# Kernel tuning notes

Measured on AMD Instinct MI355X. Metric: run time of the kernel, lower is better.

The kernel has to match this reference:

```python
import jax, jax.numpy as jnp
import numpy as np

HEAD = 8
K_DIM = 64
ROUNDS = 4
BUCKETS = 32
ACN = 1  # attend_chunk_num
SELF_VAL = -100000.0


def across(x, acn=ACN):
    """Concatenate each chunk with its acn left/right neighbor chunks (wrapping).
    x: (..., n_chunks, chunk_size, feat). Rolls along chunk axis (-3), cats along -2.
    Order matches the torch code: left chunks, self, right chunks."""
    shifts = list(range(acn, 0, -1)) + [0] + list(range(-1, -acn - 1, -1))
    return jnp.concatenate([jnp.roll(x, s, axis=-3) for s in shifts], axis=-2)


def gather_seq(src, idx):
    """src: (b,h,s,f); idx: (b,h,r,s) -> (b,h,r,s,f) (per-round permutation gather)."""
    return jnp.take_along_axis(src[:, :, None, :, :], idx[..., None], axis=-2)


def lsh_forward(x, Wq, bq, Wv, bv, Wo, bo, hash_vec):
    b, s, d = x.shape
    h, k, r = HEAD, K_DIM, ROUNDS
    qk = (x @ Wq + bq).reshape(b, s, h, k).transpose(0, 2, 1, 3)  # (b,h,s,k)
    v = (x @ Wv + bv).reshape(b, s, h, k).transpose(0, 2, 1, 3)   # (b,h,s,k)

    # --- LSH hashing: argmax over [-rot, rot] rotations ---
    rot = jnp.einsum('bhsk,hkvr->bhsvr', qk, hash_vec)
    rot = jnp.concatenate([-rot, rot], axis=-2)
    buckets = jnp.argmax(rot, axis=-2).transpose(0, 1, 3, 2)  # (b,h,r,s)

    ticker = jnp.arange(s)
    buckets = buckets * s + ticker  # stable-sort key: bucket major, position minor
    s_ticker = jnp.argsort(buckets, axis=-1)
    s_buckets = jnp.take_along_axis(buckets, s_ticker, axis=-1)
    undo = jnp.argsort(s_ticker, axis=-1)

    s_qk = gather_seq(qk, s_ticker)  # (b,h,r,s,k)
    s_v = gather_seq(v, s_ticker)
    nrm = jnp.maximum(jnp.linalg.norm(s_qk, axis=-1, keepdims=True), 1e-12)
    s_k = s_qk / nrm  # F.normalize(p=2)

    nb = BUCKETS
    cs = s // nb
    cq = s_qk.reshape(b, h, r, nb, cs, k)
    ck = s_k.reshape(b, h, r, nb, cs, k)
    cv = s_v.reshape(b, h, r, nb, cs, k)
    ct = s_ticker.reshape(b, h, r, nb, cs)

    ak = across(ck)                      # (b,h,r,nb,3cs,k)
    av = across(cv)
    at = across(ct[..., None])[..., 0]   # (b,h,r,nb,3cs)

    dots = jnp.einsum('bhrnik,bhrnjk->bhrnij', cq, ak) * (k ** -0.5)
    NEG = -jnp.finfo(dots.dtype).max

    # self-attention penalty mask
    dots = jnp.where(ct[..., :, None] == at[..., None, :], SELF_VAL, dots)

    # different-bucket mask
    bid = (s_buckets // s).reshape(b, h, r, nb, cs)
    abid = across(bid[..., None])[..., 0]
    dots = jnp.where(bid[..., :, None] != abid[..., None, :], NEG, dots)

    # duplicate count across rounds (same bucket id in any round)
    loc = (buckets // s).transpose(0, 1, 3, 2)     # (b,h,s,r)
    s_loc = gather_seq(loc, s_ticker)              # (b,h,r,s,r)
    cl = s_loc.reshape(b, h, r, nb, cs, r)
    al = across(cl)                                # (b,h,r,nb,3cs,r)
    dup = (cl[..., :, None, :] == al[..., None, :, :]).sum(-1).astype(dots.dtype)
    dup = jax.lax.stop_gradient(dup)
    dots = dots - jnp.log(dup + 1e-9)

    lse = jax.nn.logsumexp(dots, axis=-1, keepdims=True)
    p = jnp.exp(dots - lse)
    vo = jnp.einsum('bhrnij,bhrnjk->bhrnik', p, av).reshape(b, h, r, s, k)
    lse = lse.reshape(b, h, r, s)

    # unsort back to original token order
    vo = jnp.take_along_axis(vo, undo[..., None], axis=-2)
    lse = jnp.take_along_axis(lse, undo, axis=-1)

    # combine rounds with softmax over per-round logsumexp
    w = jnp.exp(lse - jax.nn.logsumexp(lse, axis=2, keepdims=True))
    out = (vo * w[..., None]).sum(axis=2)  # (b,h,s,k)
    out = out.transpose(0, 2, 1, 3).reshape(b, s, h * k)
    return out @ Wo + bo  # dropout is identity in eval


def setup_inputs() -> dict:
    key = jax.random.key(0)
    ks = jax.random.split(key, 8)
    b, s, d = 2, 2048, 512
    sc = 1.0 / np.sqrt(d)  # keep activations numerically tame
    return {
        'x': jax.random.normal(ks[0], (b, s, d), jnp.float32),
        'Wq': jax.random.normal(ks[1], (d, d), jnp.float32) * sc,
        'bq': jax.random.normal(ks[2], (d,), jnp.float32) * 0.01,
        'Wv': jax.random.normal(ks[3], (d, d), jnp.float32) * sc,
        'bv': jax.random.normal(ks[4], (d,), jnp.float32) * 0.01,
        'Wo': jax.random.normal(ks[5], (d, d), jnp.float32) * sc,
        'bo': jax.random.normal(ks[6], (d,), jnp.float32) * 0.01,
        'hash_vec': jax.random.normal(ks[7], (HEAD, K_DIM, BUCKETS // 2, ROUNDS), jnp.float32),
    }


def reference(x, Wq, bq, Wv, bv, Wo, bo, hash_vec):
    return lsh_forward(x, Wq, bq, Wv, bv, Wo, bo, hash_vec)
```

## Files before the change

kernel.cpp:

```cpp
#include <hip/hip_runtime.h>
#include <hip/hip_bf16.h>
#include <math.h>

#define WS_ 192
#define NEGF (-3.402823466e+38f)

typedef __attribute__((ext_vector_type(8))) short short8;
typedef __attribute__((ext_vector_type(4))) float f32x4;
typedef __attribute__((ext_vector_type(4))) unsigned int u32x4;

static __device__ __forceinline__ unsigned int f2bf(float f) {
    unsigned int u = __float_as_uint(f);
    return (u + 0x7FFFu + ((u >> 16) & 1u)) >> 16;
}
static __device__ __forceinline__ unsigned int packsplit(float v) {
    unsigned int h = f2bf(v);
    float hf = __uint_as_float(h << 16);
    unsigned int l = f2bf(v - hf);
    return h | (l << 16);
}
static __device__ __forceinline__ void mkfrag(uint4 a, uint4 b, short8 &h, short8 &l) {
    u32x4 hv, lv;
    hv[0] = __builtin_amdgcn_perm(a.y, a.x, 0x05040100u);
    hv[1] = __builtin_amdgcn_perm(a.w, a.z, 0x05040100u);
    hv[2] = __builtin_amdgcn_perm(b.y, b.x, 0x05040100u);
    hv[3] = __builtin_amdgcn_perm(b.w, b.z, 0x05040100u);
    lv[0] = __builtin_amdgcn_perm(a.y, a.x, 0x07060302u);
    lv[1] = __builtin_amdgcn_perm(a.w, a.z, 0x07060302u);
    lv[2] = __builtin_amdgcn_perm(b.y, b.x, 0x07060302u);
    lv[3] = __builtin_amdgcn_perm(b.w, b.z, 0x07060302u);
    h = __builtin_bit_cast(short8, hv);
    l = __builtin_bit_cast(short8, lv);
}
static __device__ __forceinline__ unsigned int cvtpk(float lo, float hi) {
    unsigned int d;
    asm("v_cvt_pk_bf16_f32 %0, %1, %2" : "=v"(d) : "v"(lo), "v"(hi));
    return d;
}
static __device__ __forceinline__ void gload_lds16(const void* g, void* l) {
    __builtin_amdgcn_global_load_lds(
        (const __attribute__((address_space(1))) void*)g,
        (__attribute__((address_space(3))) void*)l, 16, 0, 0);
}

__global__ __launch_bounds__(256) void prep_kernel(const float* __restrict__ A,
                                                   const float* __restrict__ W,
                                                   const float* __restrict__ bias,
                                                   const float* __restrict__ hv,
                                                   const float* __restrict__ Wv,
                                                   const float* __restrict__ Wo,
                                                   unsigned short* __restrict__ qkr,
                                                   float* __restrict__ scaleQ,
                                                   int* __restrict__ loc2,
                                                   unsigned int* __restrict__ xpk,
                                                   unsigned int* __restrict__ wvT,
                                                   unsigned int* __restrict__ woT) {
    __shared__ float BUF[4352];
    const int bid = blockIdx.x;
    const int tid = threadIdx.x;

    if (bid >= 512) {
        int pb = bid - 512;
        if (pb < 2048) {
            int idx = (pb * 256 + tid) * 4;
            float4 v = *(const float4*)(A + idx);
            uint4 pk = make_uint4(packsplit(v.x), packsplit(v.y),
                                  packsplit(v.z), packsplit(v.w));
            *(uint4*)(xpk + idx) = pk;
            return;
        }
        unsigned int* T = (unsigned int*)BUF;
        int wb = pb - 2048;
        const float* Wsrc = (wb < 64) ? Wv : Wo;
        unsigned int* Wdst = (wb < 64) ? wvT : woT;
        int t = wb & 63;
        int k0 = (t >> 3) * 64, n0 = (t & 7) * 64;
#pragma unroll
        for (int pass = 0; pass < 16; ++pass) {
            int i = pass * 4 + (tid >> 6);
            int j = tid & 63;
            T[j * 65 + i] = packsplit(Wsrc[(size_t)(k0 + i) * 512 + n0 + j]);
        }
        __syncthreads();
#pragma unroll
        for (int pass = 0; pass < 16; ++pass) {
            int j = pass * 4 + (tid >> 6);
            int i = tid & 63;
            Wdst[(size_t)(n0 + j) * 512 + k0 + i] = T[j * 65 + i];
        }
        return;
    }

    float* As = BUF;
    float* Ws = BUF + 2176;
    const int m0 = (bid & 63) * 64;
    const int n0 = (bid >> 6) * 64;
    const int ty = tid >> 4, tx = tid & 15;
    const int ci = tid & 7, ri = tid >> 3;
    const int wk = tid >> 4, wt = tid & 15;
    float acc[4][4] = {};
    for (int k0 = 0; k0 < 512; k0 += 32) {
#pragma unroll
        for (int h2 = 0; h2 < 2; ++h2) {
            int i = ri + h2 * 32;
            float4 a4 = *(const float4*)(A + (size_t)(m0 + i) * 512 + k0 + ci * 4);
            As[(ci * 4 + 0) * 68 + i] = a4.x;
            As[(ci * 4 + 1) * 68 + i] = a4.y;
            As[(ci * 4 + 2) * 68 + i] = a4.z;
            As[(ci * 4 + 3) * 68 + i] = a4.w;
        }
#pragma unroll
        for (int h2 = 0; h2 < 2; ++h2) {
            int kk = wk + h2 * 16;
            float4 w4 = *(const float4*)(W + (size_t)(k0 + kk) * 512 + n0 + wt * 4);
            *(float4*)(&Ws[kk * 68 + wt * 4]) = w4;
        }
        __syncthreads();
#pragma unroll
        for (int kk = 0; kk < 32; ++kk) {
            float4 a4 = *(float4*)(&As[kk * 68 + ty * 4]);
            float4 w4 = *(float4*)(&Ws[kk * 68 + tx * 4]);
            float a[4] = {a4.x, a4.y, a4.z, a4.w};
            float w[4] = {w4.x, w4.y, w4.z, w4.w};
#pragma unroll
            for (int i = 0; i < 4; ++i)
#pragma unroll
                for (int j = 0; j < 4; ++j) acc[i][j] += a[i] * w[j];
        }
        __syncthreads();
    }
    const int hh = n0 >> 6;
#pragma unroll
    for (int i = 0; i < 4; ++i) {
        int m = m0 + ty * 4 + i;
        int b = m >> 11, s = m & 2047;
        float v0 = acc[i][0] + bias[n0 + tx * 4 + 0];
        float v1 = acc[i][1] + bias[n0 + tx * 4 + 1];
        float v2 = acc[i][2] + bias[n0 + tx * 4 + 2];
        float v3 = acc[i][3] + bias[n0 + tx * 4 + 3];
        acc[i][0] = v0; acc[i][1] = v1; acc[i][2] = v2; acc[i][3] = v3;
        unsigned int h0 = f2bf(v0), h1 = f2bf(v1), h2v = f2bf(v2), h3 = f2bf(v3);
        unsigned int l0 = f2bf(v0 - __uint_as_float(h0 << 16));
        unsigned int l1 = f2bf(v1 - __uint_as_float(h1 << 16));
        unsigned int l2 = f2bf(v2 - __uint_as_float(h2v << 16));
        unsigned int l3 = f2bf(v3 - __uint_as_float(h3 << 16));
        size_t trow = ((size_t)(((b << 3) + hh) * 2048 + s)) * 128;
        *(uint2*)(qkr + trow + tx * 4) =
            make_uint2(h0 | (h1 << 16), h2v | (h3 << 16));
        *(uint2*)(qkr + trow + 64 + tx * 4) =
            make_uint2(l0 | (l1 << 16), l2 | (l3 << 16));
        float sq = v0 * v0 + v1 * v1 + v2 * v2 + v3 * v3;
        sq += __shfl_xor(sq, 1, 16); sq += __shfl_xor(sq, 2, 16);
        sq += __shfl_xor(sq, 4, 16); sq += __shfl_xor(sq, 8, 16);
        if (tx == 0)
            scaleQ[(size_t)(((b << 3) + hh) * 2048 + s)] = 0.125f / fmaxf(sqrtf(sq), 1e-12f);
    }
#pragma unroll
    for (int j = 0; j < 4; ++j) {
        int f = tx * 4 + j;
        int xm = (f & 7) << 3;
#pragma unroll
        for (int i = 0; i < 4; ++i)
            BUF[f * 68 + ((ty * 4 + i) ^ xm)] = acc[i][j];
    }
    __syncthreads();
    const float* hvb = hv + (size_t)hh * 4096 + tx * 4;
    float rt[4][4] = {};
#pragma unroll 4
    for (int f = 0; f < 64; ++f) {
        float4 q4 = *(float4*)(&BUF[f * 68 + ((ty * 4) ^ ((f & 7) << 3))]);
        float4 h4 = *(const float4*)(hvb + f * 64);
        float q[4] = {q4.x, q4.y, q4.z, q4.w};
        float hw[4] = {h4.x, h4.y, h4.z, h4.w};
#pragma unroll
        for (int i = 0; i < 4; ++i)
#pragma unroll
            for (int j = 0; j < 4; ++j) rt[i][j] += q[i] * hw[j];
    }
    __syncthreads();
#pragma unroll
    for (int i = 0; i < 4; ++i)
        *(float4*)(&BUF[(ty * 4 + i) * 68 + tx * 4]) =
            make_float4(rt[i][0], rt[i][1], rt[i][2], rt[i][3]);
    __syncthreads();
    {
        const int tok = tid >> 2, rr2 = tid & 3;
        float best = -BUF[tok * 68 + rr2];
        int bj = 0;
        for (int j = 1; j < 16; ++j) {
            float v = BUF[tok * 68 + j * 4 + rr2];
            if (-v > best) { best = -v; bj = j; }
        }
        for (int j = 0; j < 16; ++j) {
            float v = BUF[tok * 68 + j * 4 + rr2];
            if (v > best) { best = v; bj = 16 + j; }
        }
        int m = m0 + tok;
        int b = m >> 11, s = m & 2047;
        loc2[((size_t)(((b << 3) + hh) * 2048 + s)) * 4 + rr2] = bj;
    }
}

__global__ __launch_bounds__(256) void gemm_pk(const unsigned int* __restrict__ Apk,
                                               const unsigned int* __restrict__ BT,
                                               const float* __restrict__ bias,
                                               void* __restrict__ Cout, int mode) {
    __shared__ __align__(16) unsigned int As[64 * 32];
    __shared__ __align__(16) unsigned int Bs[64 * 32];
    const int m0 = blockIdx.x * 64;
    const int n0 = blockIdx.y * 64;
    const int tid = threadIdx.x;
    const int lane = tid & 63, wv = tid >> 6;
    const int lx = lane & 15, hi = lane >> 4;
    const int wbase = tid & ~63;
    f32x4 acc[4] = {{0.f,0.f,0.f,0.f},{0.f,0.f,0.f,0.f},{0.f,0.f,0.f,0.f},{0.f,0.f,0.f,0.f}};
    for (int k0 = 0; k0 < 512; k0 += 32) {
#pragma unroll
        for (int u = 0; u < 2; ++u) {
            int qi = u * 256 + tid;
            int row = qi >> 3, qd = qi & 7;
            int sq = (qd ^ (row & 7)) << 2;
            gload_lds16(Apk + (size_t)(m0 + row) * 512 + k0 + sq,
                        &As[(u * 256 + wbase) * 4]);
            gload_lds16(BT + (size_t)(n0 + row) * 512 + k0 + sq,
                        &Bs[(u * 256 + wbase) * 4]);
        }
        __syncthreads();
        int arow = wv * 16 + lx;
        uint4 a0 = *(uint4*)(&As[arow * 32 + (((2 * hi) ^ (arow & 7)) << 2)]);
        uint4 a1 = *(uint4*)(&As[arow * 32 + (((2 * hi + 1) ^ (arow & 7)) << 2)]);
        short8 Ah, Al; mkfrag(a0, a1, Ah, Al);
#pragma unroll
        for (int j = 0; j < 4; ++j) {
            int brow = j * 16 + lx;
            uint4 b0 = *(uint4*)(&Bs[brow * 32 + (((2 * hi) ^ (brow & 7)) << 2)]);
            uint4 b1 = *(uint4*)(&Bs[brow * 32 + (((2 * hi + 1) ^ (brow & 7)) << 2)]);
            short8 Bh2, Bl2; mkfrag(b0, b1, Bh2, Bl2);
            acc[j] = __builtin_amdgcn_mfma_f32_16x16x32_bf16(Ah, Bh2, acc[j], 0, 0, 0);
            acc[j] = __builtin_amdgcn_mfma_f32_16x16x32_bf16(Ah, Bl2, acc[j], 0, 0, 0);
            acc[j] = __builtin_amdgcn_mfma_f32_16x16x32_bf16(Al, Bh2, acc[j], 0, 0, 0);
        }
        __syncthreads();
    }
#pragma unroll
    for (int j = 0; j < 4; ++j) {
        int nn = n0 + j * 16 + lx;
        float bs = bias[nn];
#pragma unroll
        for (int reg = 0; reg < 4; ++reg) {
            int m = m0 + wv * 16 + hi * 4 + reg;
            float val = acc[j][reg] + bs;
            if (mode == 0) {
                int b = m >> 11, ss = m & 2047;
                int hh = nn >> 6, f = nn & 63;
                ((unsigned short*)Cout)[((size_t)(((b << 3) + hh) * 2048 + ss)) * 64 + f] =
                    (unsigned short)f2bf(val);
            } else {
                ((float*)Cout)[(size_t)m * 512 + nn] = val;
            }
        }
    }
}

__global__ __launch_bounds__(1024) void sort_kernel(const int* __restrict__ loc2,
                                                    int* __restrict__ st) {
    __shared__ int hist[32][32];
    __shared__ int off[32][32];
    __shared__ int base[32];
    const int gid = blockIdx.x;
    const int r = gid & 3, bh = gid >> 2;
    const int tid = threadIdx.x;
    const int lane = tid & 63, wvi = tid >> 6;
    const unsigned long long lower_mask =
        (lane == 0) ? 0ull : ((~0ull) >> (64 - lane));

    int myb[2], myrank[2];
#pragma unroll
    for (int si = 0; si < 2; ++si) {
        int seg = wvi * 2 + si;
        int p = seg * 64 + lane;
        int b = loc2[(size_t)(bh * 2048 + p) * 4 + r];
        myb[si] = b;
        myrank[si] = 0;
#pragma unroll 1
        for (int bkt = 0; bkt < 32; ++bkt) {
            unsigned long long m = __ballot(b == bkt);
            if (b == bkt) myrank[si] = __popcll(m & lower_mask);
            if (lane == bkt) hist[seg][bkt] = __popcll(m);
        }
    }
    __syncthreads();
    if (tid < 32) {
        int running = 0;
#pragma unroll 1
        for (int seg = 0; seg < 32; ++seg) {
            off[seg][tid] = running;
            running += hist[seg][tid];
        }
        base[tid] = running;
    }
    __syncthreads();
    if (tid == 0) {
        int acc = 0;
#pragma unroll 1
        for (int b = 0; b < 32; ++b) { int h = base[b]; base[b] = acc; acc += h; }
    }
    __syncthreads();
#pragma unroll
    for (int si = 0; si < 2; ++si) {
        int seg = wvi * 2 + si;
        int p = seg * 64 + lane;
        int b = myb[si];
        st[(size_t)gid * 2048 + base[b] + off[seg][b] + myrank[si]] = p;
    }
}

#define KSLOT(row, sl) (((row) << 6) + ((((sl) ^ ((row) & 15))) << 2))
#define PBASE 6400

__global__ __launch_bounds__(256, 3) void attn_kernel(const unsigned short* __restrict__ qkr,
                                                      const unsigned short* __restrict__ vpk,
                                                      const float* __restrict__ scaleQ,
                                                      const int* __restrict__ loc2,
                                                      const int* __restrict__ st,
                                                      float* __restrict__ lseg,
                                                      float* __restrict__ vog) {
    __shared__ __align__(16) unsigned int U[12800];
    __shared__ float scaleK[WS_];
    __shared__ int Tk[WS_];
    __shared__ int Lp[WS_];

    const int gid = blockIdx.x;
    const int n = gid & 31;
    const int r = (gid >> 5) & 3;
    const int bh = gid >> 7;
    const int tid = threadIdx.x;
    const int sbase = (bh * 4 + r) * 2048;
    const int lane = tid & 63;
    const int wv = tid >> 6;
    const int lx = lane & 15;
    const int hi = lane >> 4;

    if (tid < WS_) {
        int w = tid;
        int chunk = (n + 31 + (w >> 6)) & 31;
        int t = st[(size_t)sbase + chunk * 64 + (w & 63)];
        Tk[w] = t;
        int4 l4 = *(const int4*)(loc2 + (size_t)(bh * 2048 + t) * 4);
        Lp[w] = l4.x | (l4.y << 8) | (l4.z << 16) | (l4.w << 24);
        scaleK[w] = scaleQ[bh * 2048 + t];
    }
    __syncthreads();

#pragma unroll
    for (int it = 0; it < 12; ++it) {
        int s = it * 256 + tid;
        int row = s >> 4, sl = s & 15;
        uint4 v4 = *(const uint4*)(qkr + ((size_t)(bh * 2048 + Tk[row])) * 128 + sl * 8);
        *(uint4*)(&U[KSLOT(row, sl)]) = v4;
    }
    __syncthreads();

    const int qw = 64 + wv * 16 + lx;
    short8 Bh[2], Bl[2];
#pragma unroll
    for (int ks = 0; ks < 2; ++ks) {
        Bh[ks] = __builtin_bit_cast(short8, *(uint4*)(&U[KSLOT(qw, ks * 4 + hi)]));
        Bl[ks] = __builtin_bit_cast(short8, *(uint4*)(&U[KSLOT(qw, 8 + ks * 4 + hi)]));
    }
    f32x4 s[12];
    __builtin_amdgcn_s_setprio(1);
#pragma unroll
    for (int ct = 0; ct < 12; ++ct) {
        f32x4 acc = {0.f, 0.f, 0.f, 0.f};
#pragma unroll
        for (int ks = 0; ks < 2; ++ks) {
            int arow = ct * 16 + lx;
            short8 Ah = __builtin_bit_cast(short8, *(uint4*)(&U[KSLOT(arow, ks * 4 + hi)]));
            short8 Al = __builtin_bit_cast(short8, *(uint4*)(&U[KSLOT(arow, 8 + ks * 4 + hi)]));
            acc = __builtin_amdgcn_mfma_f32_16x16x32_bf16(Ah, Bh[ks], acc, 0, 0, 0);
            acc = __builtin_amdgcn_mfma_f32_16x16x32_bf16(Ah, Bl[ks], acc, 0, 0, 0);
            acc = __builtin_amdgcn_mfma_f32_16x16x32_bf16(Al, Bh[ks], acc, 0, 0, 0);
        }
        s[ct] = acc;
    }
    __builtin_amdgcn_s_setprio(0);

    uint4 vl0[3], vl1[3];
#pragma unroll
    for (int it = 0; it < 3; ++it) {
        int idx = it * 256 + tid;
        int pr = idx >> 3, oct = idx & 7;
        vl0[it] = *(const uint4*)(vpk + ((size_t)(bh * 2048 + Tk[pr * 2])) * 64 + oct * 8);
        vl1[it] = *(const uint4*)(vpk + ((size_t)(bh * 2048 + Tk[pr * 2 + 1])) * 64 + oct * 8);
    }
    __syncthreads();

    const int lq = Lp[qw];
    const unsigned int bmask = 0x80u << (r * 8);
    float mx = -3.0e38f;
#pragma unroll
    for (int ct = 0; ct < 12; ++ct) {
#pragma unroll
        for (int rr = 0; rr < 4; ++rr) {
            int c = ct * 16 + hi * 4 + rr;
            float val = s[ct][rr] * scaleK[c];
            unsigned int x = (unsigned int)(lq ^ Lp[c]);
            unsigned int z = ((x & 0x7f7f7f7fu) + 0x7f7f7f7fu) | x;
            unsigned int zm = ~z & 0x80808080u;
            int dup = __popc(zm);
            val = (c == qw) ? -100000.0f : val;
            val = (zm & bmask) ? val : NEGF;
            float ld = (dup < 2) ? 0.0f
                     : (dup == 2) ? 0.69314718f
                     : (dup == 3) ? 1.09861229f : 1.38629436f;
            val -= ld;
            s[ct][rr] = val;
            mx = fmaxf(mx, val);
        }
    }
    mx = fmaxf(mx, __shfl_xor(mx, 16));
    mx = fmaxf(mx, __shfl_xor(mx, 32));
    float ssum = 0.f;
#pragma unroll
    for (int ct = 0; ct < 12; ++ct)
#pragma unroll
        for (int rr = 0; rr < 4; ++rr) {
            float e = __expf(s[ct][rr] - mx);
            s[ct][rr] = e;
            ssum += e;
        }
    ssum += __shfl_xor(ssum, 16);
    ssum += __shfl_xor(ssum, 32);
    float lse = mx + __logf(ssum);
    if (hi == 0) lseg[(size_t)sbase + Tk[qw]] = lse;
    float inv = 1.0f / ssum;

#pragma unroll
    for (int it = 0; it < 3; ++it) {
        int idx = it * 256 + tid;
        int pr = idx >> 3, oct = idx & 7;
        int c0 = pr * 2;
        unsigned int aw[4] = {vl0[it].x, vl0[it].y, vl0[it].z, vl0[it].w};
        unsigned int bw[4] = {vl1[it].x, vl1[it].y, vl1[it].z, vl1[it].w};
#pragma unroll
        for (int j = 0; j < 8; ++j) {
            int f = oct * 8 + j;
            unsigned int w2 = (j & 1)
                ? __builtin_amdgcn_perm(bw[j >> 1], aw[j >> 1], 0x07060302u)
                : __builtin_amdgcn_perm(bw[j >> 1], aw[j >> 1], 0x05040100u);
            int quad = (c0 >> 3) ^ (f & 7) ^ (f >> 3);
            U[f * 100 + (quad << 2) + ((c0 & 7) >> 1)] = w2;
        }
    }
    const int q = wv * 16 + lx;
    const int pxm = (q & 3) << 3;
#pragma unroll
    for (int ct = 0; ct < 12; ++ct) {
        int po = ct * 8 + hi * 2;
        U[PBASE + q * 100 + ((po + 0) ^ pxm)] = cvtpk(s[ct][0] * inv, s[ct][1] * inv);
        U[PBASE + q * 100 + ((po + 1) ^ pxm)] = cvtpk(s[ct][2] * inv, s[ct][3] * inv);
    }
    __syncthreads();

    f32x4 o[4] = {{0.f,0.f,0.f,0.f},{0.f,0.f,0.f,0.f},{0.f,0.f,0.f,0.f},{0.f,0.f,0.f,0.f}};
    const unsigned short* Uh = (const unsigned short*)U;
    __builtin_amdgcn_s_setprio(1);
#pragma unroll
    for (int ks = 0; ks < 6; ++ks) {
        short8 P8 = *(const short8*)(Uh + PBASE * 2 + q * 200 +
                                     (((ks * 16 + hi * 4) ^ pxm) << 1));
#pragma unroll
        for (int ft = 0; ft < 4; ++ft) {
            int f = ft * 16 + lx;
            int quad = (4 * ks + hi) ^ (f & 7) ^ (f >> 3);
            short8 V8 = *(const short8*)(Uh + f * 200 + (quad << 3));
            o[ft] = __builtin_amdgcn_mfma_f32_16x16x32_bf16(V8, P8, o[ft], 0, 0, 0);
        }
    }
    __builtin_amdgcn_s_setprio(0);
    const int tko = Tk[qw];
#pragma unroll
    for (int ft = 0; ft < 4; ++ft) {
        float4 w4 = make_float4(o[ft][0], o[ft][1], o[ft][2], o[ft][3]);
        *(float4*)(vog + ((size_t)sbase + tko) * 64 + ft * 16 + hi * 4) = w4;
    }
}

__global__ __launch_bounds__(256) void combine_kernel(const float* __restrict__ vog,
                                                      const float* __restrict__ lseg,
                                                      unsigned int* __restrict__ attpk) {
    const int gid = blockIdx.x * 256 + threadIdx.x;
    const int kq = gid & 15;
    const int t = (gid >> 4) & 2047;
    const int bh = gid >> 15;
    const int b = bh >> 3, h = bh & 7;
    float l[4];
    float4 vo[4];
#pragma unroll
    for (int r = 0; r < 4; ++r) {
        l[r] = lseg[(size_t)(bh * 4 + r) * 2048 + t];
        vo[r] = *(const float4*)(vog + ((size_t)(bh * 4 + r) * 2048 + t) * 64 + kq * 4);
    }
    float m = fmaxf(fmaxf(l[0], l[1]), fmaxf(l[2], l[3]));
    float ss = expf(l[0] - m) + expf(l[1] - m) + expf(l[2] - m) + expf(l[3] - m);
    float lt = m + logf(ss);
    float o0 = 0.f, o1 = 0.f, o2 = 0.f, o3 = 0.f;
#pragma unroll
    for (int r = 0; r < 4; ++r) {
        float w = expf(l[r] - lt);
        o0 += w * vo[r].x; o1 += w * vo[r].y; o2 += w * vo[r].z; o3 += w * vo[r].w;
    }
    uint4 pk = make_uint4(packsplit(o0), packsplit(o1), packsplit(o2), packsplit(o3));
    *(uint4*)(attpk + ((size_t)(b * 2048 + t)) * 512 + h * 64 + kq * 4) = pk;
}

extern "C" void kernel_launch(void* const* d_in, const int* in_sizes, int n_in,
                              void* d_out, int out_size, void* d_ws, size_t ws_size,
                              hipStream_t stream) {
    const float* x  = (const float*)d_in[0];
    const float* Wq = (const float*)d_in[1];
    const float* bq = (const float*)d_in[2];
    const float* Wv = (const float*)d_in[3];
    const float* bv = (const float*)d_in[4];
    const float* Wo = (const float*)d_in[5];
    const float* bo = (const float*)d_in[6];
    const float* hv = (const float*)d_in[7];

    unsigned int* W = (unsigned int*)d_ws;
    float*          vog    = (float*)W;
    unsigned int*   xpk    = W + 2097152;
    unsigned short* qkr    = (unsigned short*)(W + 8388608);
    unsigned short* vpk    = (unsigned short*)(W + 10485760);
    unsigned int*   attpk  = W + 11534336;
    float*          scaleQ = (float*)(W + 13631488);
    int*            loc2   = (int*)(W + 13664256);
    int*            stbuf  = (int*)(W + 13795328);
    float*          lseg   = (float*)(W + 13926400);
    unsigned int*   wvT    = W + 14057472;
    unsigned int*   woT    = W + 14319616;

    dim3 gg(64, 8), blk(256);
    prep_kernel<<<2688, 256, 0, stream>>>(x, Wq, bq, hv, Wv, Wo,
                                          qkr, scaleQ, loc2, xpk, wvT, woT);
    gemm_pk<<<gg, blk, 0, stream>>>(xpk, wvT, bv, (void*)vpk, 0);
    sort_kernel<<<64, 1024, 0, stream>>>(loc2, stbuf);
    attn_kernel<<<2048, 256, 0, stream>>>(qkr, vpk, scaleQ, loc2, stbuf, lseg, vog);
    combine_kernel<<<2048, 256, 0, stream>>>(vog, lseg, attpk);
    gemm_pk<<<gg, blk, 0, stream>>>(attpk, woT, bo, d_out, 1);
}
```

Before: 146.8 us.

## Store split-bf16 operands as separate hi/lo planes and fuse sort into V GEMM

The packed hi|lo bf16 layout for x, Wv, Wo and the attention output becomes two separate planes per row (hi in the first 512 entries, lo in the next 512). The GEMM can then load MFMA fragments directly from LDS without per-fragment byte permutes. The bucket counting sort moves from its own kernel into the V-projection GEMM launch as extra blocks, saving one launch and letting the sort overlap the GEMM. The cost is that each sort block now handles 8 segments per wave with 256 threads instead of 1024.

```diff
diff --git a/kernel.cpp b/kernel.cpp
--- a/kernel.cpp
+++ b/kernel.cpp
@@ -7,7 +7,6 @@
 
 typedef __attribute__((ext_vector_type(8))) short short8;
 typedef __attribute__((ext_vector_type(4))) float f32x4;
-typedef __attribute__((ext_vector_type(4))) unsigned int u32x4;
 
 static __device__ __forceinline__ unsigned int f2bf(float f) {
     unsigned int u = __float_as_uint(f);
@@ -18,19 +17,6 @@
     float hf = __uint_as_float(h << 16);
     unsigned int l = f2bf(v - hf);
     return h | (l << 16);
-}
-static __device__ __forceinline__ void mkfrag(uint4 a, uint4 b, short8 &h, short8 &l) {
-    u32x4 hv, lv;
-    hv[0] = __builtin_amdgcn_perm(a.y, a.x, 0x05040100u);
-    hv[1] = __builtin_amdgcn_perm(a.w, a.z, 0x05040100u);
-    hv[2] = __builtin_amdgcn_perm(b.y, b.x, 0x05040100u);
-    hv[3] = __builtin_amdgcn_perm(b.w, b.z, 0x05040100u);
-    lv[0] = __builtin_amdgcn_perm(a.y, a.x, 0x07060302u);
-    lv[1] = __builtin_amdgcn_perm(a.w, a.z, 0x07060302u);
-    lv[2] = __builtin_amdgcn_perm(b.y, b.x, 0x07060302u);
-    lv[3] = __builtin_amdgcn_perm(b.w, b.z, 0x07060302u);
-    h = __builtin_bit_cast(short8, hv);
-    l = __builtin_bit_cast(short8, lv);
 }
 static __device__ __forceinline__ unsigned int cvtpk(float lo, float hi) {
     unsigned int d;
@@ -52,9 +38,9 @@
                                                    unsigned short* __restrict__ qkr,
                                                    float* __restrict__ scaleQ,
                                                    int* __restrict__ loc2,
-                                                   unsigned int* __restrict__ xpk,
-                                                   unsigned int* __restrict__ wvT,
-                                                   unsigned int* __restrict__ woT) {
+                                                   unsigned short* __restrict__ xpk,
+                                                   unsigned short* __restrict__ wvT,
+                                                   unsigned short* __restrict__ woT) {
     __shared__ float BUF[4352];
     const int bid = blockIdx.x;
     const int tid = threadIdx.x;
@@ -63,16 +49,22 @@
         int pb = bid - 512;
         if (pb < 2048) {
             int idx = (pb * 256 + tid) * 4;
+            int row = idx >> 9, k = idx & 511;
             float4 v = *(const float4*)(A + idx);
-            uint4 pk = make_uint4(packsplit(v.x), packsplit(v.y),
-                                  packsplit(v.z), packsplit(v.w));
-            *(uint4*)(xpk + idx) = pk;
+            unsigned int h0 = f2bf(v.x), h1 = f2bf(v.y), h2 = f2bf(v.z), h3 = f2bf(v.w);
+            unsigned int l0 = f2bf(v.x - __uint_as_float(h0 << 16));
+            unsigned int l1 = f2bf(v.y - __uint_as_float(h1 << 16));
+            unsigned int l2 = f2bf(v.z - __uint_as_float(h2 << 16));
+            unsigned int l3 = f2bf(v.w - __uint_as_float(h3 << 16));
+            size_t rb = (size_t)row * 1024 + k;
+            *(uint2*)(xpk + rb)       = make_uint2(h0 | (h1 << 16), h2 | (h3 << 16));
+            *(uint2*)(xpk + rb + 512) = make_uint2(l0 | (l1 << 16), l2 | (l3 << 16));
             return;
         }
         unsigned int* T = (unsigned int*)BUF;
         int wb = pb - 2048;
         const float* Wsrc = (wb < 64) ? Wv : Wo;
-        unsigned int* Wdst = (wb < 64) ? wvT : woT;
+        unsigned short* Wdst = (wb < 64) ? wvT : woT;
         int t = wb & 63;
         int k0 = (t >> 3) * 64, n0 = (t & 7) * 64;
 #pragma unroll
@@ -86,7 +78,10 @@
         for (int pass = 0; pass < 16; ++pass) {
             int j = pass * 4 + (tid >> 6);
             int i = tid & 63;
-            Wdst[(size_t)(n0 + j) * 512 + k0 + i] = T[j * 65 + i];
+            unsigned int pk = T[j * 65 + i];
+            size_t rb = (size_t)(n0 + j) * 1024 + k0 + i;
+            Wdst[rb]       = (unsigned short)(pk & 0xffffu);
+            Wdst[rb + 512] = (unsigned short)(pk >> 16);
         }
         return;
     }
@@ -201,41 +196,99 @@
     }
 }
 
-__global__ __launch_bounds__(256) void gemm_pk(const unsigned int* __restrict__ Apk,
-                                               const unsigned int* __restrict__ BT,
+__global__ __launch_bounds__(256) void gemm_pk(const unsigned short* __restrict__ Apk,
+                                               const unsigned short* __restrict__ BT,
                                                const float* __restrict__ bias,
-                                               void* __restrict__ Cout, int mode) {
+                                               void* __restrict__ Cout, int mode,
+                                               const int* __restrict__ loc2,
+                                               int* __restrict__ st) {
     __shared__ __align__(16) unsigned int As[64 * 32];
     __shared__ __align__(16) unsigned int Bs[64 * 32];
-    const int m0 = blockIdx.x * 64;
-    const int n0 = blockIdx.y * 64;
+    const int bid = blockIdx.x;
     const int tid = threadIdx.x;
+
+    if (bid >= 512) {
+        int gid = bid - 512;
+        int r = gid & 3, bh = gid >> 2;
+        int* hist = (int*)As;
+        int* off  = (int*)As + 1024;
+        int* base = (int*)Bs;
+        const int lane = tid & 63, wvi = tid >> 6;
+        const unsigned long long lower_mask =
+            (lane == 0) ? 0ull : ((~0ull) >> (64 - lane));
+        int myb[8], myrank[8];
+#pragma unroll
+        for (int si = 0; si < 8; ++si) {
+            int seg = wvi * 8 + si;
+            int p = seg * 64 + lane;
+            int b = loc2[(size_t)(bh * 2048 + p) * 4 + r];
+            myb[si] = b;
+            myrank[si] = 0;
+#pragma unroll 1
+            for (int bkt = 0; bkt < 32; ++bkt) {
+                unsigned long long m = __ballot(b == bkt);
+                if (b == bkt) myrank[si] = __popcll(m & lower_mask);
+                if (lane == bkt) hist[seg * 32 + bkt] = __popcll(m);
+            }
+        }
+        __syncthreads();
+        if (tid < 32) {
+            int running = 0;
+#pragma unroll 1
+            for (int seg = 0; seg < 32; ++seg) {
+                off[seg * 32 + tid] = running;
+                running += hist[seg * 32 + tid];
+            }
+            base[tid] = running;
+        }
+        __syncthreads();
+        if (tid == 0) {
+            int a2 = 0;
+#pragma unroll 1
+            for (int b = 0; b < 32; ++b) { int h = base[b]; base[b] = a2; a2 += h; }
+        }
+        __syncthreads();
+#pragma unroll
+        for (int si = 0; si < 8; ++si) {
+            int seg = wvi * 8 + si;
+            int p = seg * 64 + lane;
+            int b = myb[si];
+            st[(size_t)gid * 2048 + base[b] + off[seg * 32 + b] + myrank[si]] = p;
+        }
+        return;
+    }
+
+    const int m0 = (bid & 63) * 64;
+    const int n0 = (bid >> 6) * 64;
     const int lane = tid & 63, wv = tid >> 6;
-    const int lx = lane & 15, hi = lane >> 4;
+    const int lx = lane & 15, fg = lane >> 4;
     const int wbase = tid & ~63;
     f32x4 acc[4] = {{0.f,0.f,0.f,0.f},{0.f,0.f,0.f,0.f},{0.f,0.f,0.f,0.f},{0.f,0.f,0.f,0.f}};
     for (int k0 = 0; k0 < 512; k0 += 32) {
 #pragma unroll
         for (int u = 0; u < 2; ++u) {
             int qi = u * 256 + tid;
-            int row = qi >> 3, qd = qi & 7;
-            int sq = (qd ^ (row & 7)) << 2;
-            gload_lds16(Apk + (size_t)(m0 + row) * 512 + k0 + sq,
+            int row = qi >> 3, sl = qi & 7;
+            int ssl = sl ^ (row & 7);
+            int offp = (ssl < 4) ? (k0 + ssl * 8) : (512 + k0 + (ssl - 4) * 8);
+            gload_lds16(Apk + (size_t)(m0 + row) * 1024 + offp,
                         &As[(u * 256 + wbase) * 4]);
-            gload_lds16(BT + (size_t)(n0 + row) * 512 + k0 + sq,
+            gload_lds16(BT + (size_t)(n0 + row) * 1024 + offp,
                         &Bs[(u * 256 + wbase) * 4]);
         }
         __syncthreads();
         int arow = wv * 16 + lx;
-        uint4 a0 = *(uint4*)(&As[arow * 32 + (((2 * hi) ^ (arow & 7)) << 2)]);
-        uint4 a1 = *(uint4*)(&As[arow * 32 + (((2 * hi + 1) ^ (arow & 7)) << 2)]);
-        short8 Ah, Al; mkfrag(a0, a1, Ah, Al);
+        short8 Ah = __builtin_bit_cast(short8,
+            *(uint4*)(&As[arow * 32 + ((fg ^ (arow & 7)) << 2)]));
+        short8 Al = __builtin_bit_cast(short8,
+            *(uint4*)(&As[arow * 32 + (((4 + fg) ^ (arow & 7)) << 2)]));
 #pragma unroll
         for (int j = 0; j < 4; ++j) {
             int brow = j * 16 + lx;
-            uint4 b0 = *(uint4*)(&Bs[brow * 32 + (((2 * hi) ^ (brow & 7)) << 2)]);
-            uint4 b1 = *(uint4*)(&Bs[brow * 32 + (((2 * hi + 1) ^ (brow & 7)) << 2)]);
-            short8 Bh2, Bl2; mkfrag(b0, b1, Bh2, Bl2);
+            short8 Bh2 = __builtin_bit_cast(short8,
+                *(uint4*)(&Bs[brow * 32 + ((fg ^ (brow & 7)) << 2)]));
+            short8 Bl2 = __builtin_bit_cast(short8,
+                *(uint4*)(&Bs[brow * 32 + (((4 + fg) ^ (brow & 7)) << 2)]));
             acc[j] = __builtin_amdgcn_mfma_f32_16x16x32_bf16(Ah, Bh2, acc[j], 0, 0, 0);
             acc[j] = __builtin_amdgcn_mfma_f32_16x16x32_bf16(Ah, Bl2, acc[j], 0, 0, 0);
             acc[j] = __builtin_amdgcn_mfma_f32_16x16x32_bf16(Al, Bh2, acc[j], 0, 0, 0);
@@ -248,7 +301,7 @@
         float bs = bias[nn];
 #pragma unroll
         for (int reg = 0; reg < 4; ++reg) {
-            int m = m0 + wv * 16 + hi * 4 + reg;
+            int m = m0 + wv * 16 + fg * 4 + reg;
             float val = acc[j][reg] + bs;
             if (mode == 0) {
                 int b = m >> 11, ss = m & 2047;
@@ -259,59 +312,6 @@
                 ((float*)Cout)[(size_t)m * 512 + nn] = val;
             }
         }
-    }
-}
-
-__global__ __launch_bounds__(1024) void sort_kernel(const int* __restrict__ loc2,
-                                                    int* __restrict__ st) {
-    __shared__ int hist[32][32];
-    __shared__ int off[32][32];
-    __shared__ int base[32];
-    const int gid = blockIdx.x;
-    const int r = gid & 3, bh = gid >> 2;
-    const int tid = threadIdx.x;
-    const int lane = tid & 63, wvi = tid >> 6;
-    const unsigned long long lower_mask =
-        (lane == 0) ? 0ull : ((~0ull) >> (64 - lane));
-
-    int myb[2], myrank[2];
-#pragma unroll
-    for (int si = 0; si < 2; ++si) {
-        int seg = wvi * 2 + si;
-        int p = seg * 64 + lane;
-        int b = loc2[(size_t)(bh * 2048 + p) * 4 + r];
-        myb[si] = b;
-        myrank[si] = 0;
-#pragma unroll 1
-        for (int bkt = 0; bkt < 32; ++bkt) {
-            unsigned long long m = __ballot(b == bkt);
-            if (b == bkt) myrank[si] = __popcll(m & lower_mask);
-            if (lane == bkt) hist[seg][bkt] = __popcll(m);
-        }
-    }
-    __syncthreads();
-    if (tid < 32) {
-        int running = 0;
-#pragma unroll 1
-        for (int seg = 0; seg < 32; ++seg) {
-            off[seg][tid] = running;
-            running += hist[seg][tid];
-        }
-        base[tid] = running;
-    }
-    __syncthreads();
-    if (tid == 0) {
-        int acc = 0;
-#pragma unroll 1
-        for (int b = 0; b < 32; ++b) { int h = base[b]; base[b] = acc; acc += h; }
-    }
-    __syncthreads();
-#pragma unroll
-    for (int si = 0; si < 2; ++si) {
-        int seg = wvi * 2 + si;
-        int p = seg * 64 + lane;
-        int b = myb[si];
-        st[(size_t)gid * 2048 + base[b] + off[seg][b] + myrank[si]] = p;
     }
 }
 
@@ -489,7 +489,7 @@
 
 __global__ __launch_bounds__(256) void combine_kernel(const float* __restrict__ vog,
                                                       const float* __restrict__ lseg,
-                                                      unsigned int* __restrict__ attpk) {
+                                                      unsigned short* __restrict__ attpk) {
     const int gid = blockIdx.x * 256 + threadIdx.x;
     const int kq = gid & 15;
     const int t = (gid >> 4) & 2047;
@@ -511,8 +511,14 @@
         float w = expf(l[r] - lt);
         o0 += w * vo[r].x; o1 += w * vo[r].y; o2 += w * vo[r].z; o3 += w * vo[r].w;
     }
-    uint4 pk = make_uint4(packsplit(o0), packsplit(o1), packsplit(o2), packsplit(o3));
-    *(uint4*)(attpk + ((size_t)(b * 2048 + t)) * 512 + h * 64 + kq * 4) = pk;
+    unsigned int h0 = f2bf(o0), h1 = f2bf(o1), h2 = f2bf(o2), h3 = f2bf(o3);
+    unsigned int l0 = f2bf(o0 - __uint_as_float(h0 << 16));
+    unsigned int l1 = f2bf(o1 - __uint_as_float(h1 << 16));
+    unsigned int l2 = f2bf(o2 - __uint_as_float(h2 << 16));
+    unsigned int l3 = f2bf(o3 - __uint_as_float(h3 << 16));
+    size_t rb = ((size_t)(b * 2048 + t)) * 1024 + h * 64 + kq * 4;
+    *(uint2*)(attpk + rb)       = make_uint2(h0 | (h1 << 16), h2 | (h3 << 16));
+    *(uint2*)(attpk + rb + 512) = make_uint2(l0 | (l1 << 16), l2 | (l3 << 16));
 }
 
 extern "C" void kernel_launch(void* const* d_in, const int* in_sizes, int n_in,
@@ -529,23 +535,22 @@
 
     unsigned int* W = (unsigned int*)d_ws;
     float*          vog    = (float*)W;
-    unsigned int*   xpk    = W + 2097152;
+    unsigned short* xpk    = (unsigned short*)(W + 2097152);
     unsigned short* qkr    = (unsigned short*)(W + 8388608);
     unsigned short* vpk    = (unsigned short*)(W + 10485760);
-    unsigned int*   attpk  = W + 11534336;
+    unsigned short* attpk  = (unsigned short*)(W + 11534336);
     float*          scaleQ = (float*)(W + 13631488);
     int*            loc2   = (int*)(W + 13664256);
     int*            stbuf  = (int*)(W + 13795328);
     float*          lseg   = (float*)(W + 13926400);
-    unsigned int*   wvT    = W + 14057472;
-    unsigned int*   woT    = W + 14319616;
-
-    dim3 gg(64, 8), blk(256);
-    prep_kernel<<<2688, 256, 0, stream>>>(x, Wq, bq, hv, Wv, Wo,
+    unsigned short* wvT    = (unsigned short*)(W + 14057472);
+    unsigned short* woT    = (unsigned short*)(W + 14319616);
+
+    dim3 blk(256);
+    prep_kernel<<<2688, blk, 0, stream>>>(x, Wq, bq, hv, Wv, Wo,
                                           qkr, scaleQ, loc2, xpk, wvT, woT);
-    gemm_pk<<<gg, blk, 0, stream>>>(xpk, wvT, bv, (void*)vpk, 0);
-    sort_kernel<<<64, 1024, 0, stream>>>(loc2, stbuf);
-    attn_kernel<<<2048, 256, 0, stream>>>(qkr, vpk, scaleQ, loc2, stbuf, lseg, vog);
-    combine_kernel<<<2048, 256, 0, stream>>>(vog, lseg, attpk);
-    gemm_pk<<<gg, blk, 0, stream>>>(attpk, woT, bo, d_out, 1);
-}
+    gemm_pk<<<576, blk, 0, stream>>>(xpk, wvT, bv, (void*)vpk, 0, loc2, stbuf);
+    attn_kernel<<<2048, blk, 0, stream>>>(qkr, vpk, scaleQ, loc2, stbuf, lseg, vog);
+    combine_kernel<<<2048, blk, 0, stream>>>(vog, lseg, attpk);
+    gemm_pk<<<512, blk, 0, stream>>>(attpk, woT, bo, d_out, 1, loc2, stbuf);
+}
```

New measurement: 143.7 us. 2.1% less time.
